# Kernel tuning notes

Measured on AMD Instinct MI355X. Metric: run time of the kernel, lower is better.

Reference implementation:

```python
import jax, jax.numpy as jnp
import numpy as np

V = 50257   # vocab_size
D = 768     # d_model
NL = 4      # n_layers
DI = 1536   # d_inner = expand * d_model
DS = 16     # d_state
DC = 4      # d_conv
B = 2       # batch
L = 512     # seq_len
EPS = 1e-5  # RMSNorm eps
STD = 0.02  # init std


def setup_inputs() -> dict:
    key = jax.random.key(0)
    ks = jax.random.split(key, 8)
    idx = jax.random.randint(ks[0], (B, L), 0, V)
    emb = jax.random.normal(ks[1], (V, D), dtype=jnp.float32) * STD          # tied embedding / lm_head
    W_in = jax.random.normal(ks[2], (NL, 2 * DI, D), dtype=jnp.float32) * STD
    conv_w = jax.random.normal(ks[3], (NL, DI, 1, DC), dtype=jnp.float32) * STD  # depthwise conv [O,I/g,K]
    W_xproj = jax.random.normal(ks[4], (NL, 2 * DS + 1, DI), dtype=jnp.float32) * STD
    W_dt = jax.random.normal(ks[5], (NL, DI, 1), dtype=jnp.float32) * STD    # dt_rank = 1
    b_dt = jnp.zeros((NL, DI), dtype=jnp.float32)
    a_log = jnp.tile(jnp.log(jnp.arange(1, DS + 1, dtype=jnp.float32)), (NL, DI, 1))
    d_param = jnp.ones((NL, DI), dtype=jnp.float32)
    W_out = jax.random.normal(ks[6], (NL, D, DI), dtype=jnp.float32) * STD
    norm_w = jnp.ones((D,), dtype=jnp.float32)
    return dict(idx=idx, emb=emb, W_in=W_in, conv_w=conv_w, W_xproj=W_xproj,
                W_dt=W_dt, b_dt=b_dt, a_log=a_log, d_param=d_param,
                W_out=W_out, norm_w=norm_w)


def _mamba_block(x, W_in, conv_w, W_xproj, W_dt, b_dt, a_log, d_param, W_out):
    # in_proj + split into x, z
    xz = jnp.einsum('bld,ed->ble', x, W_in)            # [B,L,2*DI]
    xs, z = jnp.split(xz, 2, axis=-1)
    # causal depthwise conv1d (torch pads d_conv-1 both sides, keeps first L -> left pad only)
    xc = jnp.transpose(xs, (0, 2, 1))                  # [B,DI,L]
    xc = jax.lax.conv_general_dilated(xc, conv_w, window_strides=(1,),
                                      padding=[(DC - 1, 0)],
                                      feature_group_count=DI,
                                      dimension_numbers=('NCH', 'OIH', 'NCH'))
    xs = jax.nn.silu(jnp.transpose(xc, (0, 2, 1)))     # [B,L,DI]
    # selective SSM
    A = -jnp.exp(a_log)                                # [DI,DS]
    xp = jnp.einsum('bld,ed->ble', xs, W_xproj)        # [B,L,2*DS+1]
    dt_raw = xp[..., 0]                                # [B,L]
    Bp = xp[..., 1:1 + DS]                             # [B,L,DS]
    Cp = xp[..., 1 + DS:]                              # [B,L,DS]
    delta = jax.nn.softplus(dt_raw[..., None] * W_dt[:, 0] + b_dt)  # [B,L,DI]

    def step(h, inp):
        d_i, b_i, c_i, x_i = inp                       # [B,DI],[B,DS],[B,DS],[B,DI]
        a_bar = jnp.exp(d_i[:, :, None] * A)           # [B,DI,DS]
        h = a_bar * h + d_i[:, :, None] * b_i[:, None, :] * x_i[:, :, None]
        y = jnp.einsum('bn,bdn->bd', c_i, h) + d_param * x_i
        return h, y

    h0 = jnp.zeros((x.shape[0], DI, DS), dtype=x.dtype)
    seq = (jnp.moveaxis(delta, 1, 0), jnp.moveaxis(Bp, 1, 0),
           jnp.moveaxis(Cp, 1, 0), jnp.moveaxis(xs, 1, 0))
    _, ys = jax.lax.scan(step, h0, seq)
    y = jnp.moveaxis(ys, 0, 1)                         # [B,L,DI]
    y = y * jax.nn.silu(z)
    return jnp.einsum('ble,de->bld', y, W_out)         # [B,L,D]


def reference(idx, emb, W_in, conv_w, W_xproj, W_dt, b_dt, a_log, d_param, W_out, norm_w):
    x = emb[idx]                                       # [B,L,D]

    def layer(carry, p):
        w_in, c_w, w_xp, w_dt, bdt, alog, dpar, w_out = p
        out = carry + _mamba_block(carry, w_in, c_w, w_xp, w_dt, bdt, alog, dpar, w_out)
        return out, None

    x, _ = jax.lax.scan(layer, x, (W_in, conv_w, W_xproj, W_dt, b_dt, a_log, d_param, W_out))
    rms = jax.lax.rsqrt(jnp.mean(x * x, axis=-1, keepdims=True) + EPS)
    x = x * rms * norm_w
    logits = jnp.einsum('bld,vd->blv', x, emb)         # tied lm_head
    return logits
```

## Files before the change

### kernel.cpp

```cpp
#include <hip/hip_runtime.h>
#include <cstdint>

#define VV     50257
#define VPAD   50304
#define DMODEL 768
#define NLAYER 4
#define DINNER 1536
#define DSTATE 16
#define DCONV  4
#define BATCH  2
#define SEQ    512
#define MROWS  (BATCH*SEQ)

typedef unsigned short u16;
typedef __attribute__((ext_vector_type(8))) short bf16x8;
typedef __attribute__((ext_vector_type(4))) float f32x4;

__device__ __forceinline__ u16 f2bf(float f) {
  unsigned u = __float_as_uint(f);
  u += 0x7fffu + ((u >> 16) & 1u);
  return (u16)(u >> 16);
}

__device__ __forceinline__ void async16(const void* g, void* l) {
  auto gp = reinterpret_cast<const __attribute__((address_space(1))) unsigned int*>(
      reinterpret_cast<uintptr_t>(g));
  auto lp = reinterpret_cast<__attribute__((address_space(3))) unsigned int*>(
      reinterpret_cast<uintptr_t>(l));
  __builtin_amdgcn_global_load_lds(gp, lp, 16, 0, 0);
}

__global__ void prep_kern(const float* __restrict__ emb, const float* __restrict__ W_in,
                          const float* __restrict__ W_out, const int* __restrict__ idx,
                          u16* __restrict__ embbf, u16* __restrict__ winbf,
                          u16* __restrict__ woutbf, float* __restrict__ xf,
                          u16* __restrict__ xbf) {
  const int E4  = VPAD * DMODEL / 4;
  const int W14 = NLAYER * 2 * DINNER * DMODEL / 4;
  const int W24 = NLAYER * DMODEL * DINNER / 4;
  const int X4  = MROWS * DMODEL / 4;
  const int TOT = E4 + W14 + W24 + X4;
  int i = blockIdx.x * blockDim.x + threadIdx.x;
  const int stride = gridDim.x * blockDim.x;
  for (; i < TOT; i += stride) {
    if (i < E4) {
      ushort4 o;
      if (i < VV * DMODEL / 4) {
        float4 v = *(const float4*)(emb + (long)i * 4);
        o.x = f2bf(v.x); o.y = f2bf(v.y); o.z = f2bf(v.z); o.w = f2bf(v.w);
      } else { o.x = 0; o.y = 0; o.z = 0; o.w = 0; }
      *(ushort4*)(embbf + (long)i * 4) = o;
    } else if (i < E4 + W14) {
      const int j = i - E4;
      float4 v = *(const float4*)(W_in + (long)j * 4);
      ushort4 o; o.x = f2bf(v.x); o.y = f2bf(v.y); o.z = f2bf(v.z); o.w = f2bf(v.w);
      *(ushort4*)(winbf + (long)j * 4) = o;
    } else if (i < E4 + W14 + W24) {
      const int j = i - E4 - W14;
      float4 v = *(const float4*)(W_out + (long)j * 4);
      ushort4 o; o.x = f2bf(v.x); o.y = f2bf(v.y); o.z = f2bf(v.z); o.w = f2bf(v.w);
      *(ushort4*)(woutbf + (long)j * 4) = o;
    } else {
      const int j = i - E4 - W14 - W24;
      const int r = j / (DMODEL / 4);
      const int c = (j % (DMODEL / 4)) * 4;
      const int id = idx[r];
      float4 v = *(const float4*)(emb + (long)id * DMODEL + c);
      *(float4*)(xf + (long)r * DMODEL + c) = v;
      ushort4 o; o.x = f2bf(v.x); o.y = f2bf(v.y); o.z = f2bf(v.z); o.w = f2bf(v.w);
      *(ushort4*)(xbf + (long)r * DMODEL + c) = o;
    }
  }
}

template<bool GUARDN, bool XSWZ>
__global__ __launch_bounds__(256) void gemm3_kern(
    const u16* __restrict__ A, const u16* __restrict__ B,
    float* __restrict__ C, int M, int N, int K, int lda, int ldb)
{
  __shared__ u16 As[3][128 * 32];
  __shared__ u16 Bs[3][128 * 32];
  int bx, by;
  if (XSWZ) {
    const int nt = gridDim.x >> 3;
    const int t = (blockIdx.x & 7) * nt + (blockIdx.x >> 3);
    bx = t & 7; by = t >> 3;
  } else { bx = blockIdx.x; by = blockIdx.y; }
  const int koff = blockIdx.z * K;
  const long coff = (long)blockIdx.z * M * N;

  const int tid  = threadIdx.x;
  const int wave = tid >> 6;
  const int lane = tid & 63;
  const int wr = wave >> 1, wc = wave & 1;
  const int m0 = bx * 128;
  const int n0 = by * 128;

  const int srow = wave * 32 + (lane >> 2);
  const int sblk = ((lane & 3) ^ ((lane >> 3) & 3)) * 8;

  f32x4 acc[4][4];
#pragma unroll
  for (int i = 0; i < 4; ++i)
#pragma unroll
    for (int j = 0; j < 4; ++j) acc[i][j] = (f32x4){0.f, 0.f, 0.f, 0.f};

  const int arow = wr * 64 + (lane & 15);
  const int brow = wc * 64 + (lane & 15);
  const int sa   = (((lane >> 4) ^ ((lane >> 1) & 3)) << 3);

  const int KT = K / 32;
  auto stage = [&](int kt) {
    const int slot = kt % 3;
    const long kcol = (long)koff + kt * 32;
#pragma unroll
    for (int j = 0; j < 2; ++j) {
      async16(A + (long)(m0 + srow + j * 16) * lda + kcol + sblk,
              (char*)(As[slot]) + (wave * 32 + j * 16) * 64);
      async16(B + (long)(n0 + srow + j * 16) * ldb + kcol + sblk,
              (char*)(Bs[slot]) + (wave * 32 + j * 16) * 64);
    }
  };

  stage(0);
  stage(1);
  for (int t = 0; t < KT; ++t) {
    if (t + 2 < KT) {
      stage(t + 2);
      asm volatile("s_waitcnt vmcnt(8)" ::: "memory");
    } else if (t + 2 == KT) {
      asm volatile("s_waitcnt vmcnt(4)" ::: "memory");
    } else {
      asm volatile("s_waitcnt vmcnt(0)" ::: "memory");
    }
    __builtin_amdgcn_s_barrier();
    asm volatile("" ::: "memory");

    const int slot = t % 3;
    const u16* as = As[slot];
    const u16* bs = Bs[slot];
    bf16x8 af[4], bv[4];
#pragma unroll
    for (int i = 0; i < 4; ++i) af[i] = *(const bf16x8*)(as + (arow + 16 * i) * 32 + sa);
#pragma unroll
    for (int j = 0; j < 4; ++j) bv[j] = *(const bf16x8*)(bs + (brow + 16 * j) * 32 + sa);

    __builtin_amdgcn_s_setprio(1);
#pragma unroll
    for (int i = 0; i < 4; ++i)
#pragma unroll
      for (int j = 0; j < 4; ++j)
        acc[i][j] = __builtin_amdgcn_mfma_f32_16x16x32_bf16(af[i], bv[j], acc[i][j], 0, 0, 0);
    __builtin_amdgcn_s_setprio(0);

    asm volatile("" ::: "memory");
    __builtin_amdgcn_s_barrier();
    asm volatile("" ::: "memory");
  }

  const int rbase = m0 + wr * 64 + ((lane >> 4) << 2);
  const int cbase = n0 + wc * 64 + (lane & 15);
#pragma unroll
  for (int j = 0; j < 4; ++j) {
    const int col = cbase + j * 16;
    if (GUARDN && col >= N) continue;
#pragma unroll
    for (int i = 0; i < 4; ++i) {
#pragma unroll
      for (int r = 0; r < 4; ++r) {
        const int row = rbase + i * 16 + r;
        C[coff + (long)row * N + col] = acc[i][j][r];
      }
    }
  }
}

__global__ __launch_bounds__(256) void redout_kern(const float* __restrict__ part,
                                                   float* __restrict__ xf,
                                                   u16* __restrict__ xbf) {
  const int i = blockIdx.x * blockDim.x + threadIdx.x;
  if (i >= MROWS * DMODEL / 4) return;
  const int stride4 = MROWS * DMODEL / 4;
  float4 s = ((const float4*)part)[i];
  float4 p1 = ((const float4*)part)[i + stride4];
  float4 p2 = ((const float4*)part)[i + 2 * stride4];
  float4 p3 = ((const float4*)part)[i + 3 * stride4];
  float4 x = ((const float4*)xf)[i];
  s.x += p1.x + p2.x + p3.x + x.x;
  s.y += p1.y + p2.y + p3.y + x.y;
  s.z += p1.z + p2.z + p3.z + x.z;
  s.w += p1.w + p2.w + p3.w + x.w;
  ((float4*)xf)[i] = s;
  ushort4 o; o.x = f2bf(s.x); o.y = f2bf(s.y); o.z = f2bf(s.z); o.w = f2bf(s.w);
  ((ushort4*)xbf)[i] = o;
}

__global__ __launch_bounds__(256) void convxproj_kern(
    const float* __restrict__ xz, const float* __restrict__ cw,
    const float* __restrict__ Wx, const float* __restrict__ wdt,
    const float* __restrict__ bdt,
    float* __restrict__ xs, float* __restrict__ dlt, float* __restrict__ bc)
{
  __shared__ float sx[DINNER];
  __shared__ float sxp[40];
  const int row = blockIdx.x;
  const int t = row & (SEQ - 1);
  const int tid = threadIdx.x;

  for (int c = tid; c < DINNER; c += 256) {
    const float* w = cw + c * DCONV;
    float a = 0.f;
#pragma unroll
    for (int k = 0; k < DCONV; ++k) {
      const int tt = t - (DCONV - 1) + k;
      if (tt >= 0) a += w[k] * xz[(long)(row - (DCONV - 1) + k) * (2 * DINNER) + c];
    }
    const float s = a / (1.f + __expf(-a));
    sx[c] = s;
    xs[(long)row * DINNER + c] = s;
  }
  __syncthreads();

  const int wv = tid >> 6, lane = tid & 63;
  for (int e = wv; e < 2 * DSTATE + 1; e += 4) {
    const float* We = Wx + (long)e * DINNER;
    float p = 0.f;
    for (int d = lane; d < DINNER; d += 64) p += sx[d] * We[d];
#pragma unroll
    for (int off = 32; off; off >>= 1) p += __shfl_xor(p, off, 64);
    if (lane == 0) sxp[e] = p;
  }
  __syncthreads();
  const float dtr = sxp[0];
  for (int d = tid; d < DINNER; d += 256) {
    float v = dtr * wdt[d] + bdt[d];
    float sp = (v > 15.f) ? v : log1pf(__expf(v));
    dlt[(long)row * DINNER + d] = sp;
  }
  if (tid < 2 * DSTATE) bc[(long)row * (2 * DSTATE) + tid] = sxp[1 + tid];
}

__global__ __launch_bounds__(128) void scan_kern(
    const float* __restrict__ dlt, const float* __restrict__ bc,
    const float* __restrict__ xs, const float* __restrict__ xz,
    const float* __restrict__ alog, const float* __restrict__ dpar,
    u16* __restrict__ ybf)
{
  __shared__ float sh_h[16][8][DSTATE];
  __shared__ float sh_s[16][8];
  const int tid = threadIdx.x;
  const int ch = tid & 7, chunk = tid >> 3;
  const int ch_abs = blockIdx.x * 8 + ch;
  const int b = ch_abs / DINNER, d = ch_abs % DINNER;
  float An[DSTATE];
#pragma unroll
  for (int n = 0; n < DSTATE; ++n) An[n] = -__expf(alog[(long)d * DSTATE + n]);
  const int r0 = b * SEQ + chunk * 32;

  float h[DSTATE];
#pragma unroll
  for (int n = 0; n < DSTATE; ++n) h[n] = 0.f;
  float ssum = 0.f;
  for (int s = 0; s < 32; ++s) {
    const int row = r0 + s;
    const float dl = dlt[(long)row * DINNER + d];
    const float xv = xs[(long)row * DINNER + d];
    const float dx = dl * xv;
    const float4* bp = (const float4*)(bc + (long)row * (2 * DSTATE));
    float Bv[DSTATE];
    *(float4*)&Bv[0]  = bp[0]; *(float4*)&Bv[4]  = bp[1];
    *(float4*)&Bv[8]  = bp[2]; *(float4*)&Bv[12] = bp[3];
    ssum += dl;
#pragma unroll
    for (int n = 0; n < DSTATE; ++n) h[n] = __expf(dl * An[n]) * h[n] + dx * Bv[n];
  }
#pragma unroll
  for (int n = 0; n < DSTATE; ++n) sh_h[chunk][ch][n] = h[n];
  sh_s[chunk][ch] = ssum;
  __syncthreads();

  {
    const int n2 = tid & 15, ch2 = tid >> 4;
    const int d2 = (blockIdx.x * 8 + ch2) % DINNER;
    const float A2 = -__expf(alog[(long)d2 * DSTATE + n2]);
    float carry = 0.f;
    for (int c = 0; c < 16; ++c) {
      const float hl = sh_h[c][ch2][n2];
      sh_h[c][ch2][n2] = carry;
      carry = __expf(A2 * sh_s[c][ch2]) * carry + hl;
    }
  }
  __syncthreads();

#pragma unroll
  for (int n = 0; n < DSTATE; ++n) h[n] = sh_h[chunk][ch][n];
  const float dp = dpar[d];
  for (int s = 0; s < 32; ++s) {
    const int row = r0 + s;
    const float dl = dlt[(long)row * DINNER + d];
    const float xv = xs[(long)row * DINNER + d];
    const float dx = dl * xv;
    const float4* bp = (const float4*)(bc + (long)row * (2 * DSTATE));
    float Bv[DSTATE], Cv[DSTATE];
    *(float4*)&Bv[0]  = bp[0]; *(float4*)&Bv[4]  = bp[1];
    *(float4*)&Bv[8]  = bp[2]; *(float4*)&Bv[12] = bp[3];
    *(float4*)&Cv[0]  = bp[4]; *(float4*)&Cv[4]  = bp[5];
    *(float4*)&Cv[8]  = bp[6]; *(float4*)&Cv[12] = bp[7];
    float y = 0.f;
#pragma unroll
    for (int n = 0; n < DSTATE; ++n) {
      const float hn = __expf(dl * An[n]) * h[n] + dx * Bv[n];
      h[n] = hn;
      y += Cv[n] * hn;
    }
    y += dp * xv;
    const float zz = xz[(long)row * (2 * DINNER) + DINNER + d];
    const float o = y * (zz / (1.f + __expf(-zz)));
    ybf[(long)row * DINNER + d] = f2bf(o);
  }
}

__global__ __launch_bounds__(256) void rmsnorm_kern(const float* __restrict__ x,
                                                    const float* __restrict__ nw,
                                                    u16* __restrict__ xnbf) {
  const int row = blockIdx.x, tid = threadIdx.x;
  const float* xr = x + (long)row * DMODEL;
  float p = 0.f;
#pragma unroll
  for (int k = 0; k < 3; ++k) { float v = xr[tid + k * 256]; p += v * v; }
#pragma unroll
  for (int off = 32; off; off >>= 1) p += __shfl_xor(p, off, 64);
  __shared__ float red[4];
  __shared__ float s_rms;
  const int wv = tid >> 6, lane = tid & 63;
  if (lane == 0) red[wv] = p;
  __syncthreads();
  if (tid == 0) {
    float tsum = red[0] + red[1] + red[2] + red[3];
    s_rms = rsqrtf(tsum / (float)DMODEL + 1e-5f);
  }
  __syncthreads();
  const float r = s_rms;
#pragma unroll
  for (int k = 0; k < 3; ++k) {
    const int dd = tid + k * 256;
    xnbf[(long)row * DMODEL + dd] = f2bf(xr[dd] * r * nw[dd]);
  }
}

extern "C" void kernel_launch(void* const* d_in, const int* in_sizes, int n_in,
                              void* d_out, int out_size, void* d_ws, size_t ws_size,
                              hipStream_t stream)
{
  (void)in_sizes; (void)n_in; (void)out_size; (void)ws_size;
  const int*   idx   = (const int*)  d_in[0];
  const float* emb   = (const float*)d_in[1];
  const float* W_in  = (const float*)d_in[2];
  const float* convw = (const float*)d_in[3];
  const float* W_xp  = (const float*)d_in[4];
  const float* W_dt  = (const float*)d_in[5];
  const float* b_dt  = (const float*)d_in[6];
  const float* a_log = (const float*)d_in[7];
  const float* d_par = (const float*)d_in[8];
  const float* W_out = (const float*)d_in[9];
  const float* normw = (const float*)d_in[10];
  float* out = (float*)d_out;

  char* ws = (char*)d_ws;
  size_t off = 0;
  auto alloc = [&](size_t bytes) -> void* {
    void* p = ws + off;
    off += (bytes + 255) & ~(size_t)255;
    return p;
  };
  u16*   embbf  = (u16*)  alloc((size_t)VPAD * DMODEL * 2);
  u16*   winbf  = (u16*)  alloc((size_t)NLAYER * 2 * DINNER * DMODEL * 2);
  u16*   woutbf = (u16*)  alloc((size_t)NLAYER * DMODEL * DINNER * 2);
  float* xf     = (float*)alloc((size_t)MROWS * DMODEL * 4);
  u16*   xbf    = (u16*)  alloc((size_t)MROWS * DMODEL * 2);
  float* xz     = (float*)alloc((size_t)MROWS * 2 * DINNER * 4);
  float* xs     = (float*)alloc((size_t)MROWS * DINNER * 4);
  float* dlt    = (float*)alloc((size_t)MROWS * DINNER * 4);
  float* bc     = (float*)alloc((size_t)MROWS * 2 * DSTATE * 4);
  u16*   ybf    = (u16*)  alloc((size_t)MROWS * DINNER * 2);
  u16*   xnbf   = (u16*)  alloc((size_t)MROWS * DMODEL * 2);
  float* part   = (float*)alloc((size_t)4 * MROWS * DMODEL * 4);

  prep_kern<<<2048, 256, 0, stream>>>(emb, W_in, W_out, idx, embbf, winbf, woutbf, xf, xbf);

  for (int l = 0; l < NLAYER; ++l) {
    gemm3_kern<false, true><<<8 * (2 * DINNER / 128), 256, 0, stream>>>(
        xbf, winbf + (size_t)l * 2 * DINNER * DMODEL, xz,
        MROWS, 2 * DINNER, DMODEL, DMODEL, DMODEL);
    convxproj_kern<<<MROWS, 256, 0, stream>>>(
        xz, convw + (size_t)l * DINNER * DCONV,
        W_xp + (size_t)l * (2 * DSTATE + 1) * DINNER,
        W_dt + (size_t)l * DINNER, b_dt + (size_t)l * DINNER, xs, dlt, bc);
    scan_kern<<<BATCH * DINNER / 8, 128, 0, stream>>>(
        dlt, bc, xs, xz, a_log + (size_t)l * DINNER * DSTATE, d_par + (size_t)l * DINNER, ybf);
    gemm3_kern<false, true><<<dim3(8 * (DMODEL / 128), 1, 4), 256, 0, stream>>>(
        ybf, woutbf + (size_t)l * DMODEL * DINNER, part,
        MROWS, DMODEL, DINNER / 4, DINNER, DINNER);
    redout_kern<<<MROWS * DMODEL / 4 / 256, 256, 0, stream>>>(part, xf, xbf);
  }
  rmsnorm_kern<<<MROWS, 256, 0, stream>>>(xf, normw, xnbf);
  gemm3_kern<true, true><<<8 * (VPAD / 128), 256, 0, stream>>>(
      xnbf, embbf, out, MROWS, VV, DMODEL, DMODEL, DMODEL);
}
```

Baseline: 918.8 us.

## Add 256x256-tile 8-wave pipelined GEMM for the tied lm_head projection

Replaces the 128x128 GEMM used for the vocab-sized logits projection with a new kernel that uses 256x256 tiles, 8 waves, double-buffered LDS with XOR swizzle, interleaved async loads and MFMA phases, and XCD-aware block remapping. The vocab padding grows to a multiple of 256 so the new tile fits. The larger tile is meant to raise arithmetic intensity and overlap global loads with MFMA in this dominant GEMM. In exchange it uses 128KB of LDS per block and relies on hand-tuned waitcnt counts, which makes it fragile if the prep kernel does not zero the enlarged padding.

```diff
diff --git a/kernel.cpp b/kernel.cpp
--- a/kernel.cpp
+++ b/kernel.cpp
@@ -2,7 +2,7 @@
 #include <cstdint>
 
 #define VV     50257
-#define VPAD   50304
+#define VPAD   50432
 #define DMODEL 768
 #define NLAYER 4
 #define DINNER 1536
@@ -175,6 +175,165 @@
   }
 }
 
+__global__ __launch_bounds__(512, 2) void gemm8_kern(
+    const u16* __restrict__ A, const u16* __restrict__ B,
+    float* __restrict__ C, int N, int K, int lda, int ldb)
+{
+  __shared__ u16 lds[2][2][256 * 64];
+  const int tid = threadIdx.x;
+  const int wave = tid >> 6;
+  const int lane = tid & 63;
+  const int wm = wave >> 2, wn = wave & 3;
+
+  const int nwg = gridDim.x;
+  const int q = nwg >> 3, r = nwg & 7;
+  const int xcd = blockIdx.x & 7;
+  const int t = (xcd < r ? xcd * (q + 1) : r * (q + 1) + (xcd - r) * q) + (blockIdx.x >> 3);
+  const int m0 = (t & 3) * 256;
+  const int n0 = (t >> 2) * 256;
+
+  const int NT = K / 64;
+  const int NI = NT / 2;
+
+  const int sblk = (((lane & 7) ^ (lane >> 3)) << 3);
+  auto stage = [&](int buf, int ab, int half, int kt) {
+    const u16* Mat = ab ? B : A;
+    const int ld = ab ? ldb : lda;
+    const int tb = ab ? n0 : m0;
+#pragma unroll
+    for (int j = 0; j < 2; ++j) {
+      const int rloc = half * 128 + j * 64 + wave * 8;
+      async16(Mat + (long)(tb + rloc + (lane >> 3)) * ld + kt * 64 + sblk,
+              (char*)&lds[buf][ab][0] + (rloc << 7));
+    }
+  };
+
+  bf16x8 af[4][2], bl[2][2], bh[2][2];
+  const int aq = lane >> 4;
+  auto readA = [&](int buf, int half) {
+#pragma unroll
+    for (int mf = 0; mf < 4; ++mf) {
+      const int rr = half * 128 + wm * 64 + mf * 16 + (lane & 15);
+#pragma unroll
+      for (int ks = 0; ks < 2; ++ks) {
+        const int q2 = ks * 4 + aq;
+        af[mf][ks] = *(const bf16x8*)(&lds[buf][0][0] + rr * 64 + ((q2 ^ (rr & 7)) << 3));
+      }
+    }
+  };
+  auto readB = [&](int buf, int half, bf16x8 (&bf)[2][2]) {
+#pragma unroll
+    for (int nf = 0; nf < 2; ++nf) {
+      const int rr = half * 128 + wn * 32 + nf * 16 + (lane & 15);
+#pragma unroll
+      for (int ks = 0; ks < 2; ++ks) {
+        const int q2 = ks * 4 + aq;
+        bf[nf][ks] = *(const bf16x8*)(&lds[buf][1][0] + rr * 64 + ((q2 ^ (rr & 7)) << 3));
+      }
+    }
+  };
+
+  f32x4 acc[8][4];
+#pragma unroll
+  for (int i = 0; i < 8; ++i)
+#pragma unroll
+    for (int j = 0; j < 4; ++j) acc[i][j] = (f32x4){0.f, 0.f, 0.f, 0.f};
+
+#define MFMA16(QM, QN, BF)                                                        \
+  __builtin_amdgcn_s_setprio(1);                                                  \
+  _Pragma("unroll")                                                               \
+  for (int mf = 0; mf < 4; ++mf)                                                  \
+    _Pragma("unroll")                                                             \
+    for (int nf = 0; nf < 2; ++nf)                                                \
+      _Pragma("unroll")                                                           \
+      for (int ks = 0; ks < 2; ++ks)                                              \
+        acc[(QM)*4+mf][(QN)*2+nf] = __builtin_amdgcn_mfma_f32_16x16x32_bf16(      \
+            af[mf][ks], BF[nf][ks], acc[(QM)*4+mf][(QN)*2+nf], 0, 0, 0);          \
+  __builtin_amdgcn_s_setprio(0);
+
+#define BAR()  asm volatile("" ::: "memory"); __builtin_amdgcn_s_barrier(); asm volatile("" ::: "memory")
+#define LGKM0() asm volatile("s_waitcnt lgkmcnt(0)" ::: "memory")
+
+  stage(0, 0, 0, 0); stage(0, 1, 0, 0); stage(0, 1, 1, 0);
+  stage(0, 0, 1, 0); stage(1, 0, 0, 1); stage(1, 1, 0, 1);
+  asm volatile("s_waitcnt vmcnt(8)" ::: "memory");
+  BAR();
+
+  for (int it = 0; it < NI; ++it) {
+    const int kt = it * 2;
+    const bool last = (it == NI - 1);
+    readA(0, 0); readB(0, 0, bl);
+    stage(1, 0, 1, kt + 1);
+    asm volatile("s_waitcnt vmcnt(6)" ::: "memory");
+    BAR(); LGKM0();
+    MFMA16(0, 0, bl);
+    BAR();
+    readB(0, 1, bh);
+    stage(1, 1, 1, kt + 1);
+    BAR(); LGKM0();
+    MFMA16(0, 1, bh);
+    BAR();
+    readA(0, 1);
+    if (!last) stage(0, 0, 0, kt + 2);
+    BAR(); LGKM0();
+    MFMA16(1, 0, bl);
+    BAR();
+    if (!last) { stage(0, 1, 0, kt + 2);
+      asm volatile("s_waitcnt vmcnt(8)" ::: "memory");
+    } else {
+      asm volatile("s_waitcnt vmcnt(4)" ::: "memory");
+    }
+    BAR();
+    MFMA16(1, 1, bh);
+    BAR();
+    readA(1, 0); readB(1, 0, bl);
+    if (!last) { stage(0, 0, 1, kt + 2);
+      asm volatile("s_waitcnt vmcnt(6)" ::: "memory");
+    } else {
+      asm volatile("s_waitcnt vmcnt(0)" ::: "memory");
+    }
+    BAR(); LGKM0();
+    MFMA16(0, 0, bl);
+    BAR();
+    readB(1, 1, bh);
+    if (!last) stage(0, 1, 1, kt + 2);
+    BAR(); LGKM0();
+    MFMA16(0, 1, bh);
+    BAR();
+    readA(1, 1);
+    if (!last) stage(1, 0, 0, kt + 3);
+    BAR(); LGKM0();
+    MFMA16(1, 0, bl);
+    BAR();
+    if (!last) { stage(1, 1, 0, kt + 3);
+      asm volatile("s_waitcnt vmcnt(8)" ::: "memory");
+    }
+    BAR();
+    MFMA16(1, 1, bh);
+    if (!last) { BAR(); }
+  }
+
+#pragma unroll
+  for (int qm = 0; qm < 2; ++qm)
+#pragma unroll
+    for (int mf = 0; mf < 4; ++mf)
+#pragma unroll
+      for (int qn = 0; qn < 2; ++qn)
+#pragma unroll
+        for (int nf = 0; nf < 2; ++nf) {
+          const int col = n0 + qn * 128 + wn * 32 + nf * 16 + (lane & 15);
+          if (col >= N) continue;
+          const int row0 = m0 + qm * 128 + wm * 64 + mf * 16 + ((lane >> 4) << 2);
+          const f32x4 v = acc[qm * 4 + mf][qn * 2 + nf];
+#pragma unroll
+          for (int rr2 = 0; rr2 < 4; ++rr2)
+            C[(long)(row0 + rr2) * N + col] = v[rr2];
+        }
+#undef MFMA16
+#undef BAR
+#undef LGKM0
+}
+
 __global__ __launch_bounds__(256) void redout_kern(const float* __restrict__ part,
                                                    float* __restrict__ xf,
                                                    u16* __restrict__ xbf) {
@@ -404,6 +563,6 @@
     redout_kern<<<MROWS * DMODEL / 4 / 256, 256, 0, stream>>>(part, xf, xbf);
   }
   rmsnorm_kern<<<MROWS, 256, 0, stream>>>(xf, normw, xnbf);
-  gemm3_kern<true, true><<<8 * (VPAD / 128), 256, 0, stream>>>(
-      xnbf, embbf, out, MROWS, VV, DMODEL, DMODEL, DMODEL);
-}
+  gemm8_kern<<<4 * (VPAD / 256), 512, 0, stream>>>(
+      xnbf, embbf, out, VV, DMODEL, DMODEL, DMODEL);
+}
```

New measurement: 896.3 us. 2.5% less time.
